# Kernel tuning notes

Measured on AMD Instinct MI355X. Metric: run time of the kernel, lower is better.

The kernel has to match this reference:

```python
import jax, jax.numpy as jnp
import numpy as np

EPS = 1e-5

def _lin(x, w, b):
    return x @ w + b

def _ln(x, scale, bias):
    m = jnp.mean(x, axis=-1, keepdims=True)
    v = jnp.var(x, axis=-1, keepdims=True)
    return (x - m) / jnp.sqrt(v + EPS) * scale + bias

def setup_inputs() -> dict:
    key = jax.random.key(0)
    B, N, F, OUT, TRI = 4, 128, 128, 128, 8
    ks = iter(jax.random.split(key, 64))
    def lin_params(fan_in, fan_out):
        s = 1.0 / np.sqrt(fan_in)
        w = jax.random.uniform(next(ks), (fan_in, fan_out), minval=-s, maxval=s, dtype=jnp.float32)
        b = jax.random.uniform(next(ks), (fan_out,), minval=-s, maxval=s, dtype=jnp.float32)
        return w, b
    inp = {}
    inp['node_fts'] = jax.random.normal(next(ks), (B, N, F), dtype=jnp.float32)
    inp['edge_fts'] = jax.random.normal(next(ks), (B, N, N, F), dtype=jnp.float32)
    inp['graph_fts'] = jax.random.normal(next(ks), (B, F), dtype=jnp.float32)
    inp['hidden'] = jax.random.normal(next(ks), (B, N, F), dtype=jnp.float32)
    inp['adj_matrix'] = jax.random.randint(next(ks), (B, N, N), 0, 2, dtype=jnp.int32)
    inp['m1_w'], inp['m1_b'] = lin_params(2 * F, OUT)
    inp['m2_w'], inp['m2_b'] = lin_params(2 * F, OUT)
    inp['me_w'], inp['me_b'] = lin_params(F, OUT)
    inp['mg_w'], inp['mg_b'] = lin_params(F, OUT)
    inp['mlp1_w'], inp['mlp1_b'] = lin_params(OUT, OUT)
    inp['mlp2_w'], inp['mlp2_b'] = lin_params(OUT, OUT)
    inp['o1_w'], inp['o1_b'] = lin_params(2 * F, OUT)
    inp['o2_w'], inp['o2_b'] = lin_params(OUT, OUT)
    inp['t1_w'], inp['t1_b'] = lin_params(2 * F, TRI)
    inp['t2_w'], inp['t2_b'] = lin_params(2 * F, TRI)
    inp['te1_w'], inp['te1_b'] = lin_params(F, TRI)
    inp['te2_w'], inp['te2_b'] = lin_params(F, TRI)
    inp['te3_w'], inp['te3_b'] = lin_params(F, TRI)
    inp['tg_w'], inp['tg_b'] = lin_params(F, TRI)
    inp['o3_w'], inp['o3_b'] = lin_params(TRI, OUT)
    inp['norm_scale'] = jnp.ones((OUT,), dtype=jnp.float32)
    inp['norm_bias'] = jnp.zeros((OUT,), dtype=jnp.float32)
    return inp

def reference(node_fts, edge_fts, graph_fts, hidden, adj_matrix,
              m1_w, m1_b, m2_w, m2_b, me_w, me_b, mg_w, mg_b,
              mlp1_w, mlp1_b, mlp2_w, mlp2_b,
              o1_w, o1_b, o2_w, o2_b,
              t1_w, t1_b, t2_w, t2_b,
              te1_w, te1_b, te2_w, te2_b, te3_w, te3_b,
              tg_w, tg_b, o3_w, o3_b, norm_scale, norm_bias):
    z = jnp.concatenate([node_fts, hidden], axis=-1)          # [B,N,2F]
    msg_1 = _lin(z, m1_w, m1_b)                                # [B,N,H]
    msg_2 = _lin(z, m2_w, m2_b)
    msg_e = _lin(edge_fts, me_w, me_b)                         # [B,N,N,H]
    msg_g = _lin(graph_fts, mg_w, mg_b)                        # [B,H]
    msgs = msg_1[:, None, :, :] + msg_2[:, :, None, :] + msg_e + msg_g[:, None, None, :]
    # msg_mlp: ReLU -> Linear -> ReLU -> Linear
    msgs = _lin(jax.nn.relu(_lin(jax.nn.relu(msgs), mlp1_w, mlp1_b)), mlp2_w, mlp2_b)
    # triplet messages (note: original code reuses t_1 for tri_3 -- faithful)
    tri_1 = _lin(z, t1_w, t1_b)                                # [B,N,T]
    tri_2 = _lin(z, t2_w, t2_b)
    tri_3 = _lin(z, t1_w, t1_b)
    tri_e_1 = _lin(edge_fts, te1_w, te1_b)                     # [B,N,N,T]
    tri_e_2 = _lin(edge_fts, te2_w, te2_b)
    tri_e_3 = _lin(edge_fts, te3_w, te3_b)
    tri_g = _lin(graph_fts, tg_w, tg_b)                        # [B,T]
    triplets = (tri_1[:, :, None, None, :] + tri_2[:, None, :, None, :]
                + tri_3[:, None, None, :, :]
                + tri_e_1[:, :, :, None, :] + tri_e_2[:, :, None, :, :]
                + tri_e_3[:, None, :, :, :]
                + tri_g[:, None, None, None, :])               # [B,N,N,N,T]
    tri_msgs = _lin(jnp.max(triplets, axis=1), o3_w, o3_b)     # [B,N,N,OUT]
    tri_msgs = _ln(jax.nn.relu(tri_msgs), norm_scale, norm_bias)
    # masked max aggregation
    maxarg = jnp.where(adj_matrix[..., None] == 1, msgs, -1e9)
    msgs_agg = jnp.max(maxarg, axis=1)                         # [B,N,H]
    out = jax.nn.relu(_lin(z, o1_w, o1_b) + _lin(msgs_agg, o2_w, o2_b))
    out = _ln(out, norm_scale, norm_bias)
    return out, tri_msgs
```

## Files before the change

### kernel.cpp

```cpp
#include <hip/hip_runtime.h>
#include <hip/hip_bf16.h>
#include <cstddef>
#include <cstdint>
#include <cstring>

typedef __attribute__((ext_vector_type(8))) short bf16x8;
typedef __attribute__((ext_vector_type(4))) float f32x4;
typedef unsigned short ushort_t;

__device__ __forceinline__ ushort_t f2b(float f) {
    uint32_t x = __float_as_uint(f);
    uint32_t r = (x + 0x7FFFu + ((x >> 16) & 1u)) >> 16;
    return (ushort_t)r;
}
__device__ __forceinline__ float b2f(ushort_t u) {
    return __uint_as_float(((uint32_t)u) << 16);
}
__device__ __forceinline__ uint32_t pk2(float x, float y) {
    __hip_bfloat162 h = __float22bfloat162_rn(float2{x, y});
    uint32_t u;
    __builtin_memcpy(&u, &h, 4);
    return u;
}

__global__ void prep_kernel(const float* __restrict__ m1_w, const float* __restrict__ m2_w,
                            const float* __restrict__ o1_w, const float* __restrict__ t1_w,
                            const float* __restrict__ t2_w,
                            const float* __restrict__ me_w, const float* __restrict__ mlp1_w,
                            const float* __restrict__ mlp2_w,
                            const float* __restrict__ te1_w, const float* __restrict__ te2_w,
                            const float* __restrict__ te3_w,
                            const float* __restrict__ graph_fts,
                            const float* __restrict__ mg_w, const float* __restrict__ mg_b,
                            const float* __restrict__ m1_b,
                            const float* __restrict__ tg_w, const float* __restrict__ t2_b,
                            const float* __restrict__ tg_b,
                            ushort_t* __restrict__ Wnt,
                            ushort_t* __restrict__ Wme, ushort_t* __restrict__ Wm1,
                            ushort_t* __restrict__ Wm2, ushort_t* __restrict__ TEt,
                            float* __restrict__ G1, float* __restrict__ TG) {
    int idx = blockIdx.x * 256 + threadIdx.x;
    if (idx < 106496) {
        int o = idx >> 8, k = idx & 255;
        float v = 0.0f;
        if (o < 128)       v = m1_w[k * 128 + o];
        else if (o < 256)  v = m2_w[k * 128 + (o - 128)];
        else if (o < 384)  v = o1_w[k * 128 + (o - 256)];
        else if (o < 392)  v = t1_w[k * 8 + (o - 384)];
        else if (o < 400)  v = t2_w[k * 8 + (o - 392)];
        Wnt[idx] = f2b(v);
    } else if (idx < 122880) {
        int t = idx - 106496, o = t >> 7, h = t & 127;
        Wme[t] = f2b(me_w[h * 128 + o]);
    } else if (idx < 139264) {
        int t = idx - 122880, o = t >> 7, h = t & 127;
        Wm1[t] = f2b(mlp1_w[h * 128 + o]);
    } else if (idx < 155648) {
        int t = idx - 139264, o = t >> 7, h = t & 127;
        Wm2[t] = f2b(mlp2_w[h * 128 + o]);
    } else if (idx < 159744) {
        int t = idx - 155648, c = t >> 7, h = t & 127;
        float v = 0.0f;
        if (c < 8)       v = te1_w[h * 8 + c];
        else if (c < 16) v = te2_w[h * 8 + (c - 8)];
        else if (c < 24) v = te3_w[h * 8 + (c - 16)];
        TEt[t] = f2b(v);
    } else if (idx < 160256) {
        int t = idx - 159744, b = t >> 7, h = t & 127;
        float a = m1_b[h] + mg_b[h];
        #pragma unroll 4
        for (int k = 0; k < 128; k++) a = fmaf(graph_fts[b * 128 + k], mg_w[k * 128 + h], a);
        G1[t] = a;
    } else if (idx < 160288) {
        int t = idx - 160256, b = t >> 3, tt = t & 7;
        float a = t2_b[tt] + tg_b[tt];
        #pragma unroll 4
        for (int k = 0; k < 128; k++) a = fmaf(graph_fts[b * 128 + k], tg_w[k * 8 + tt], a);
        TG[t] = a;
    }
}

__global__ __launch_bounds__(256)
void node_gemm(const float* __restrict__ node_fts, const float* __restrict__ hidden,
               const ushort_t* __restrict__ Wnt,
               const float* __restrict__ G1, const float* __restrict__ m2_b,
               const float* __restrict__ o1_b, const float* __restrict__ t1_b,
               const float* __restrict__ TG,
               float* __restrict__ M1, float* __restrict__ M2, float* __restrict__ O1z,
               float* __restrict__ T1v, float* __restrict__ TT2) {
    __shared__ ushort_t Zs[32 * 256];
    char* Zb = (char*)Zs;
    const int tid = threadIdx.x;
    const int blk = blockIdx.x;
    const int b = blk >> 2, q = blk & 3;
    const int row0 = b * 128 + q * 32;
    const int w = tid >> 6, l = tid & 63, g = l >> 4, lq = l & 15;

    const float4* nsrc = reinterpret_cast<const float4*>(node_fts + (size_t)row0 * 128);
    const float4* hsrc = reinterpret_cast<const float4*>(hidden + (size_t)row0 * 128);
    #pragma unroll
    for (int p = 0; p < 8; p++) {
        int idx = tid + p * 256;
        int r = idx >> 6, c4 = idx & 63;
        float4 v = (c4 < 32) ? nsrc[r * 32 + c4] : hsrc[r * 32 + (c4 - 32)];
        uint2 pk;
        pk.x = pk2(v.x, v.y);
        pk.y = pk2(v.z, v.w);
        *reinterpret_cast<uint2*>(Zb + r * 512 + (((c4 >> 1) ^ (r & 7)) << 4) + (c4 & 1) * 8) = pk;
    }
    __syncthreads();

    for (int mt = w; mt < 26; mt += 4) {
        f32x4 acc0 = (f32x4){0.f, 0.f, 0.f, 0.f};
        f32x4 acc1 = (f32x4){0.f, 0.f, 0.f, 0.f};
        const ushort_t* arow = Wnt + (size_t)(mt * 16 + lq) * 256;
        #pragma unroll
        for (int ks = 0; ks < 8; ks++) {
            bf16x8 a = *reinterpret_cast<const bf16x8*>(arow + ks * 32 + g * 8);
            int j0 = lq, j1 = 16 + lq;
            bf16x8 b0 = *reinterpret_cast<const bf16x8*>(Zb + j0 * 512 + (((ks * 4 + g) ^ (j0 & 7)) << 4));
            bf16x8 b1 = *reinterpret_cast<const bf16x8*>(Zb + j1 * 512 + (((ks * 4 + g) ^ (j1 & 7)) << 4));
            acc0 = __builtin_amdgcn_mfma_f32_16x16x32_bf16(a, b0, acc0, 0, 0, 0);
            acc1 = __builtin_amdgcn_mfma_f32_16x16x32_bf16(a, b1, acc1, 0, 0, 0);
        }
        #pragma unroll
        for (int half = 0; half < 2; half++) {
            const f32x4 acc = half ? acc1 : acc0;
            const int grow = row0 + half * 16 + lq;
            #pragma unroll
            for (int c = 0; c < 4; c++) {
                int o = mt * 16 + g * 4 + c;
                float v = acc[c];
                if (o < 128)       M1[(size_t)grow * 128 + o] = v + G1[b * 128 + o];
                else if (o < 256)  M2[(size_t)grow * 128 + (o - 128)] = v + m2_b[o - 128];
                else if (o < 384)  O1z[(size_t)grow * 128 + (o - 256)] = v + o1_b[o - 256];
                else if (o < 392)  T1v[(size_t)grow * 8 + (o - 384)] = v + t1_b[o - 384];
                else if (o < 400)  TT2[(size_t)grow * 8 + (o - 392)] = v + TG[b * 8 + (o - 392)];
            }
        }
    }
}

__device__ __forceinline__ void mmv(const ushort_t* __restrict__ Wt, const char* Xa,
                                    f32x4 acc[2][4], int o_blk, int j_blk, int g, int lq) {
    #pragma unroll
    for (int ks = 0; ks < 4; ks++) {
        bf16x8 a[2], bb[4];
        #pragma unroll
        for (int m = 0; m < 2; m++)
            a[m] = *reinterpret_cast<const bf16x8*>(Wt + (size_t)(o_blk + m * 16 + lq) * 128 + ks * 32 + g * 8);
        #pragma unroll
        for (int n = 0; n < 4; n++) {
            int j = j_blk + n * 16 + lq;
            bb[n] = *reinterpret_cast<const bf16x8*>(Xa + j * 256 + (((ks * 4 + g) ^ (j & 7)) << 4));
        }
        #pragma unroll
        for (int m = 0; m < 2; m++)
            #pragma unroll
            for (int n = 0; n < 4; n++)
                acc[m][n] = __builtin_amdgcn_mfma_f32_16x16x32_bf16(a[m], bb[n], acc[m][n], 0, 0, 0);
    }
}

__global__ __launch_bounds__(512, 4)
void edge_kernel(const float* __restrict__ edge_fts,
                 const ushort_t* __restrict__ Wme, const float* __restrict__ me_b,
                 const ushort_t* __restrict__ Wm1, const float* __restrict__ mlp1_b,
                 const ushort_t* __restrict__ Wm2, const float* __restrict__ mlp2_b,
                 const ushort_t* __restrict__ TEt,
                 const float* __restrict__ te1_b, const float* __restrict__ te2_b,
                 const float* __restrict__ te3_b,
                 const float* __restrict__ M1,  const float* __restrict__ M2,
                 const float* __restrict__ T1v, const float* __restrict__ TT2,
                 ushort_t* __restrict__ msgsM, float* __restrict__ T1buf,
                 float* __restrict__ T2buf, float* __restrict__ E3buf) {
    __shared__ ushort_t Xs[2][16384];
    char* X0 = (char*)Xs[0];
    char* X1 = (char*)Xs[1];
    const int tid = threadIdx.x;
    const int b  = blockIdx.x >> 7;
    const int ie = blockIdx.x & 127;
    const int w = tid >> 6, l = tid & 63, g = l >> 4, lq = l & 15;
    const int o_blk = (w & 3) * 32, j_blk = (w >> 2) * 64;

    const float4* esrc = reinterpret_cast<const float4*>(edge_fts + (size_t)(b * 128 + ie) * 16384);
    #pragma unroll
    for (int p = 0; p < 8; p++) {
        int idx = tid + p * 512;
        int r = idx >> 5, c4 = idx & 31;
        float4 v = esrc[idx];
        uint2 pk;
        pk.x = pk2(v.x, v.y);
        pk.y = pk2(v.z, v.w);
        *reinterpret_cast<uint2*>(X0 + r * 256 + (((c4 >> 1) ^ (r & 7)) << 4) + (c4 & 1) * 8) = pk;
    }
    __syncthreads();

    {
        const int m_te = w & 1;
        const int jq = (w >> 1) & 3;
        const ushort_t* At = TEt + m_te * 16 * 128;
        f32x4 acc2[2];
        #pragma unroll
        for (int n = 0; n < 2; n++) acc2[n] = (f32x4){0.f, 0.f, 0.f, 0.f};
        #pragma unroll
        for (int ks = 0; ks < 4; ks++) {
            bf16x8 a = *reinterpret_cast<const bf16x8*>(At + lq * 128 + ks * 32 + g * 8);
            #pragma unroll
            for (int n = 0; n < 2; n++) {
                int j = jq * 32 + n * 16 + lq;
                bf16x8 bbv = *reinterpret_cast<const bf16x8*>(X0 + j * 256 + (((ks * 4 + g) ^ (j & 7)) << 4));
                acc2[n] = __builtin_amdgcn_mfma_f32_16x16x32_bf16(a, bbv, acc2[n], 0, 0, 0);
            }
        }
        if (m_te == 0) {
            if (g < 2) {
                int t0 = g * 4;
                const float4 eb = *reinterpret_cast<const float4*>(te1_b + t0);
                const float4 tv = *reinterpret_cast<const float4*>(T1v + (size_t)(b * 128 + ie) * 8 + t0);
                #pragma unroll
                for (int n = 0; n < 2; n++) {
                    int j = jq * 32 + n * 16 + lq;
                    float4 o4 = make_float4(acc2[n][0] + eb.x + tv.x, acc2[n][1] + eb.y + tv.y,
                                            acc2[n][2] + eb.z + tv.z, acc2[n][3] + eb.w + tv.w);
                    *reinterpret_cast<float4*>(T1buf + ((size_t)(b * 128 + j) * 128 + ie) * 8 + t0) = o4;
                }
            } else {
                int t0 = g * 4 - 8;
                const float4 eb = *reinterpret_cast<const float4*>(te2_b + t0);
                #pragma unroll
                for (int n = 0; n < 2; n++) {
                    int j = jq * 32 + n * 16 + lq;
                    float4 o4 = make_float4(acc2[n][0] + eb.x, acc2[n][1] + eb.y,
                                            acc2[n][2] + eb.z, acc2[n][3] + eb.w);
                    *reinterpret_cast<float4*>(T2buf + ((size_t)(b * 128 + ie) * 128 + j) * 8 + t0) = o4;
                }
            }
        } else if (g < 2) {
            int t0 = g * 4;
            const float4 eb = *reinterpret_cast<const float4*>(te3_b + t0);
            const float4 t2v = *reinterpret_cast<const float4*>(TT2 + (size_t)(b * 128 + ie) * 8 + t0);
            #pragma unroll
            for (int n = 0; n < 2; n++) {
                int j = jq * 32 + n * 16 + lq;
                const float4 t3v = *reinterpret_cast<const float4*>(T1v + (size_t)(b * 128 + j) * 8 + t0);
                float4 o4 = make_float4(acc2[n][0] + eb.x + t2v.x + t3v.x,
                                        acc2[n][1] + eb.y + t2v.y + t3v.y,
                                        acc2[n][2] + eb.z + t2v.z + t3v.z,
                                        acc2[n][3] + eb.w + t2v.w + t3v.w);
                *reinterpret_cast<float4*>(E3buf + ((size_t)(b * 128 + ie) * 128 + j) * 8 + t0) = o4;
            }
        }
    }

    f32x4 acc[2][4];

    #pragma unroll
    for (int m = 0; m < 2; m++)
        #pragma unroll
        for (int n = 0; n < 4; n++) acc[m][n] = (f32x4){0.f, 0.f, 0.f, 0.f};
    mmv(Wme, X0, acc, o_blk, j_blk, g, lq);
    {
        #pragma unroll
        for (int m = 0; m < 2; m++) {
            int o0 = o_blk + m * 16 + g * 4;
            const float4 eb = *reinterpret_cast<const float4*>(me_b + o0);
            const float4 m2 = *reinterpret_cast<const float4*>(M2 + (size_t)(b * 128 + ie) * 128 + o0);
            float4 bc = make_float4(eb.x + m2.x, eb.y + m2.y, eb.z + m2.z, eb.w + m2.w);
            #pragma unroll
            for (int n = 0; n < 4; n++) {
                int j = j_blk + n * 16 + lq;
                const float4 m1 = *reinterpret_cast<const float4*>(M1 + (size_t)(b * 128 + j) * 128 + o0);
                float r0 = fmaxf(acc[m][n][0] + bc.x + m1.x, 0.f);
                float r1 = fmaxf(acc[m][n][1] + bc.y + m1.y, 0.f);
                float r2 = fmaxf(acc[m][n][2] + bc.z + m1.z, 0.f);
                float r3 = fmaxf(acc[m][n][3] + bc.w + m1.w, 0.f);
                uint2 pk;
                pk.x = pk2(r0, r1);
                pk.y = pk2(r2, r3);
                *reinterpret_cast<uint2*>(X1 + j * 256 + ((((o0 >> 3) ^ (j & 7))) << 4) + (o0 & 7) * 2) = pk;
            }
        }
        __syncthreads();
    }

    #pragma unroll
    for (int m = 0; m < 2; m++)
        #pragma unroll
        for (int n = 0; n < 4; n++) acc[m][n] = (f32x4){0.f, 0.f, 0.f, 0.f};
    mmv(Wm1, X1, acc, o_blk, j_blk, g, lq);
    {
        #pragma unroll
        for (int m = 0; m < 2; m++) {
            int o0 = o_blk + m * 16 + g * 4;
            const float4 bb = *reinterpret_cast<const float4*>(mlp1_b + o0);
            #pragma unroll
            for (int n = 0; n < 4; n++) {
                int j = j_blk + n * 16 + lq;
                float r0 = fmaxf(acc[m][n][0] + bb.x, 0.f);
                float r1 = fmaxf(acc[m][n][1] + bb.y, 0.f);
                float r2 = fmaxf(acc[m][n][2] + bb.z, 0.f);
                float r3 = fmaxf(acc[m][n][3] + bb.w, 0.f);
                uint2 pk;
                pk.x = pk2(r0, r1);
                pk.y = pk2(r2, r3);
                *reinterpret_cast<uint2*>(X0 + j * 256 + ((((o0 >> 3) ^ (j & 7))) << 4) + (o0 & 7) * 2) = pk;
            }
        }
        __syncthreads();
    }

    #pragma unroll
    for (int m = 0; m < 2; m++)
        #pragma unroll
        for (int n = 0; n < 4; n++) acc[m][n] = (f32x4){0.f, 0.f, 0.f, 0.f};
    mmv(Wm2, X0, acc, o_blk, j_blk, g, lq);
    {
        #pragma unroll
        for (int m = 0; m < 2; m++) {
            int o0 = o_blk + m * 16 + g * 4;
            const float4 bb = *reinterpret_cast<const float4*>(mlp2_b + o0);
            #pragma unroll
            for (int n = 0; n < 4; n++) {
                int j = j_blk + n * 16 + lq;
                float r0 = acc[m][n][0] + bb.x;
                float r1 = acc[m][n][1] + bb.y;
                float r2 = acc[m][n][2] + bb.z;
                float r3 = acc[m][n][3] + bb.w;
                uint2 pk;
                pk.x = pk2(r0, r1);
                pk.y = pk2(r2, r3);
                *reinterpret_cast<uint2*>(X1 + j * 256 + ((((o0 >> 3) ^ (j & 7))) << 4) + (o0 & 7) * 2) = pk;
            }
        }
        __syncthreads();
    }

    {
        #pragma unroll
        for (int p = 0; p < 4; p++) {
            int idx = tid + p * 512;
            int r = idx >> 4, sc = idx & 15;
            uint4 v = *reinterpret_cast<const uint4*>(X1 + r * 256 + sc * 16);
            int logical = sc ^ (r & 7);
            *reinterpret_cast<uint4*>(msgsM + ((size_t)(b * 128 + r) * 128 + ie) * 128 + logical * 8) = v;
        }
    }
}

__global__ __launch_bounds__(256)
void agg_out_kernel(const ushort_t* __restrict__ msgsM, const int* __restrict__ adj,
                    const float* __restrict__ O1z,
                    const float* __restrict__ o2_w, const float* __restrict__ o2_b,
                    const float* __restrict__ scale, const float* __restrict__ bias,
                    float* __restrict__ out) {
    __shared__ float aggs[4][128];
    __shared__ float fagg[128];
    __shared__ float red[2][2];
    const int b = blockIdx.x >> 7, j = blockIdx.x & 127;
    const int t = threadIdx.x;
    const int wv = t >> 6, ln = t & 63;
    const ushort_t* msrc = msgsM + (size_t)(b * 128 + j) * 16384;
    const int* arow = adj + b * 16384 + j;
    float a0 = -1e9f, a1 = -1e9f;
    #pragma unroll 8
    for (int s = 0; s < 32; s++) {
        const int i = s * 4 + wv;
        uint32_t u = *reinterpret_cast<const uint32_t*>(msrc + i * 128 + ln * 2);
        bool m = (arow[i * 128] == 1);
        float x0 = b2f((ushort_t)(u & 0xffffu));
        float x1 = b2f((ushort_t)(u >> 16));
        a0 = m ? fmaxf(a0, x0) : a0;
        a1 = m ? fmaxf(a1, x1) : a1;
    }
    aggs[wv][ln * 2]     = a0;
    aggs[wv][ln * 2 + 1] = a1;
    __syncthreads();
    if (t < 128)
        fagg[t] = fmaxf(fmaxf(aggs[0][t], aggs[1][t]), fmaxf(aggs[2][t], aggs[3][t]));
    __syncthreads();

    float v = 0.0f;
    if (t < 128) {
        float val = o2_b[t] + O1z[(size_t)(b * 128 + j) * 128 + t];
        #pragma unroll 4
        for (int k = 0; k < 128; k++) val = fmaf(fagg[k], o2_w[k * 128 + t], val);
        v = fmaxf(val, 0.0f);
    }
    float s = v, s2 = v * v;
    #pragma unroll
    for (int off = 32; off >= 1; off >>= 1) {
        s += __shfl_down(s, off, 64);
        s2 += __shfl_down(s2, off, 64);
    }
    if (t < 128 && (t & 63) == 0) { red[t >> 6][0] = s; red[t >> 6][1] = s2; }
    __syncthreads();
    if (t < 128) {
        const float tot = red[0][0] + red[1][0];
        const float tot2 = red[0][1] + red[1][1];
        const float mean = tot * (1.0f / 128.0f);
        const float var = tot2 * (1.0f / 128.0f) - mean * mean;
        const float rstd = rsqrtf(var + 1e-5f);
        out[(size_t)(b * 128 + j) * 128 + t] = (v - mean) * rstd * scale[t] + bias[t];
    }
}

__global__ __launch_bounds__(512)
void tri_kernel(const float* __restrict__ T1buf, const float* __restrict__ T2buf,
                const float* __restrict__ E3buf, const float* __restrict__ o3_w,
                const float* __restrict__ o3_b, const float* __restrict__ scale,
                const float* __restrict__ bias, float* __restrict__ tri_out) {
    __shared__ __align__(16) float T1s[1024];
    __shared__ __align__(16) float E3s[1024];
    __shared__ __align__(16) float o3s[1024];
    __shared__ __align__(16) float Ps[4][128][8];
    const int b = blockIdx.x >> 7, jf = blockIdx.x & 127;
    const int tid = threadIdx.x;
    if (tid < 256) {
        reinterpret_cast<float4*>(T1s)[tid] =
            reinterpret_cast<const float4*>(T1buf + (size_t)(b * 128 + jf) * 1024)[tid];
        reinterpret_cast<float4*>(o3s)[tid] = reinterpret_cast<const float4*>(o3_w)[tid];
    } else {
        int t2 = tid - 256;
        reinterpret_cast<float4*>(E3s)[t2] =
            reinterpret_cast<const float4*>(E3buf + (size_t)(b * 128 + jf) * 1024)[t2];
    }
    __syncthreads();

    {
        const int kf = tid & 127, ih = tid >> 7;
        float a8[8];
        #pragma unroll
        for (int t = 0; t < 8; t++) a8[t] = -3.0e38f;
        const float4* t2p = reinterpret_cast<const float4*>(T2buf + (size_t)b * 131072);
        #pragma unroll 4
        for (int ii = 0; ii < 32; ++ii) {
            const int i = ih * 32 + ii;
            const float4 p = t2p[(i * 128 + kf) * 2];
            const float4 q = t2p[(i * 128 + kf) * 2 + 1];
            const float* t1r = &T1s[i * 8];
            a8[0] = fmaxf(a8[0], t1r[0] + p.x);
            a8[1] = fmaxf(a8[1], t1r[1] + p.y);
            a8[2] = fmaxf(a8[2], t1r[2] + p.z);
            a8[3] = fmaxf(a8[3], t1r[3] + p.w);
            a8[4] = fmaxf(a8[4], t1r[4] + q.x);
            a8[5] = fmaxf(a8[5], t1r[5] + q.y);
            a8[6] = fmaxf(a8[6], t1r[6] + q.z);
            a8[7] = fmaxf(a8[7], t1r[7] + q.w);
        }
        #pragma unroll
        for (int t = 0; t < 8; t++) Ps[ih][kf][t] = a8[t];
    }
    __syncthreads();

    const int w = tid >> 6, l = tid & 63;
    const float ob0 = o3_b[l],     ob1 = o3_b[l + 64];
    const float sc0 = scale[l],    sc1 = scale[l + 64];
    const float bi0 = bias[l],     bi1 = bias[l + 64];
    for (int kk = 0; kk < 16; ++kk) {
        const int kf = w * 16 + kk;
        float m8[8];
        #pragma unroll
        for (int t = 0; t < 8; t++)
            m8[t] = fmaxf(fmaxf(Ps[0][kf][t], Ps[1][kf][t]),
                          fmaxf(Ps[2][kf][t], Ps[3][kf][t])) + E3s[kf * 8 + t];
        float v0 = ob0, v1 = ob1;
        #pragma unroll
        for (int t = 0; t < 8; t++) {
            v0 = fmaf(m8[t], o3s[t * 128 + l], v0);
            v1 = fmaf(m8[t], o3s[t * 128 + l + 64], v1);
        }
        v0 = fmaxf(v0, 0.0f);
        v1 = fmaxf(v1, 0.0f);
        float s = v0 + v1, s2 = v0 * v0 + v1 * v1;
        #pragma unroll
        for (int off = 32; off >= 1; off >>= 1) {
            s  += __shfl_xor(s, off, 64);
            s2 += __shfl_xor(s2, off, 64);
        }
        const float mean = s * (1.0f / 128.0f);
        const float var = s2 * (1.0f / 128.0f) - mean * mean;
        const float rstd = rsqrtf(var + 1e-5f);
        float* dst = tri_out + (size_t)((b * 128 + jf) * 128 + kf) * 128;
        dst[l]      = (v0 - mean) * rstd * sc0 + bi0;
        dst[l + 64] = (v1 - mean) * rstd * sc1 + bi1;
    }
}

extern "C" void kernel_launch(void* const* d_in, const int* in_sizes, int n_in,
                              void* d_out, int out_size, void* d_ws, size_t ws_size,
                              hipStream_t stream) {
    const float* node_fts  = (const float*)d_in[0];
    const float* edge_fts  = (const float*)d_in[1];
    const float* graph_fts = (const float*)d_in[2];
    const float* hidden    = (const float*)d_in[3];
    const int*   adj       = (const int*)d_in[4];
    const float* m1_w = (const float*)d_in[5],  *m1_b = (const float*)d_in[6];
    const float* m2_w = (const float*)d_in[7],  *m2_b = (const float*)d_in[8];
    const float* me_w = (const float*)d_in[9],  *me_b = (const float*)d_in[10];
    const float* mg_w = (const float*)d_in[11], *mg_b = (const float*)d_in[12];
    const float* mlp1_w = (const float*)d_in[13], *mlp1_b = (const float*)d_in[14];
    const float* mlp2_w = (const float*)d_in[15], *mlp2_b = (const float*)d_in[16];
    const float* o1_w = (const float*)d_in[17], *o1_b = (const float*)d_in[18];
    const float* o2_w = (const float*)d_in[19], *o2_b = (const float*)d_in[20];
    const float* t1_w = (const float*)d_in[21], *t1_b = (const float*)d_in[22];
    const float* t2_w = (const float*)d_in[23], *t2_b = (const float*)d_in[24];
    const float* te1_w = (const float*)d_in[25], *te1_b = (const float*)d_in[26];
    const float* te2_w = (const float*)d_in[27], *te2_b = (const float*)d_in[28];
    const float* te3_w = (const float*)d_in[29], *te3_b = (const float*)d_in[30];
    const float* tg_w = (const float*)d_in[31], *tg_b = (const float*)d_in[32];
    const float* o3_w = (const float*)d_in[33], *o3_b = (const float*)d_in[34];
    const float* norm_scale = (const float*)d_in[35];
    const float* norm_bias  = (const float*)d_in[36];

    char* w8 = (char*)d_ws;
    float*    M1    = (float*)(w8 + 0);
    float*    M2    = (float*)(w8 + 262144);
    float*    O1z   = (float*)(w8 + 524288);
    float*    T1v   = (float*)(w8 + 786432);
    float*    TT2   = (float*)(w8 + 802816);
    ushort_t* Wme   = (ushort_t*)(w8 + 819200);
    ushort_t* Wm1   = (ushort_t*)(w8 + 851968);
    ushort_t* Wm2   = (ushort_t*)(w8 + 884736);
    ushort_t* TEt   = (ushort_t*)(w8 + 917504);
    ushort_t* msgsM = (ushort_t*)(w8 + 925696);
    float*    T1buf = (float*)(w8 + 17702912);
    float*    T2buf = (float*)(w8 + 19800064);
    float*    E3buf = (float*)(w8 + 21897216);
    ushort_t* Wnt   = (ushort_t*)(w8 + 23994368);
    float*    G1    = (float*)(w8 + 24207360);
    float*    TG    = (float*)(w8 + 24209408);

    float* out_p  = (float*)d_out;
    float* tri_p  = (float*)d_out + 65536;

    prep_kernel<<<627, 256, 0, stream>>>(m1_w, m2_w, o1_w, t1_w, t2_w,
                                         me_w, mlp1_w, mlp2_w, te1_w, te2_w, te3_w,
                                         graph_fts, mg_w, mg_b, m1_b, tg_w, t2_b, tg_b,
                                         Wnt, Wme, Wm1, Wm2, TEt, G1, TG);
    node_gemm<<<16, 256, 0, stream>>>(node_fts, hidden, Wnt, G1, m2_b, o1_b, t1_b, TG,
                                      M1, M2, O1z, T1v, TT2);
    edge_kernel<<<512, 512, 0, stream>>>(edge_fts, Wme, me_b, Wm1, mlp1_b, Wm2, mlp2_b,
                                         TEt, te1_b, te2_b, te3_b,
                                         M1, M2, T1v, TT2, msgsM, T1buf, T2buf, E3buf);
    agg_out_kernel<<<512, 256, 0, stream>>>(msgsM, adj, O1z, o2_w, o2_b,
                                            norm_scale, norm_bias, out_p);
    tri_kernel<<<512, 512, 0, stream>>>(T1buf, T2buf, E3buf, o3_w, o3_b,
                                        norm_scale, norm_bias, tri_p);
}
```

Measured before the change: 109.8 us.

## Fuse masked max aggregation and output layer into edge kernel via column-major edge tiling

Each edge_kernel block now handles one target column jf across all source rows i instead of one source row. The block therefore holds every message needed for the masked max over i in shared memory. It runs the aggregation, the o2 projection and the layernorm in place, which removes the 16 MB bf16 msgs round trip to global memory and the separate agg_out launch. Edge feature loads become strided per row (512 B chunks), and node_gemm is split into twice as many blocks across output-column halves for more parallelism.

```diff
diff --git a/kernel.cpp b/kernel.cpp
--- a/kernel.cpp
+++ b/kernel.cpp
@@ -92,7 +92,8 @@
     char* Zb = (char*)Zs;
     const int tid = threadIdx.x;
     const int blk = blockIdx.x;
-    const int b = blk >> 2, q = blk & 3;
+    const int rowblk = blk >> 1, colh = blk & 1;
+    const int b = rowblk >> 2, q = rowblk & 3;
     const int row0 = b * 128 + q * 32;
     const int w = tid >> 6, l = tid & 63, g = l >> 4, lq = l & 15;
 
@@ -110,7 +111,7 @@
     }
     __syncthreads();
 
-    for (int mt = w; mt < 26; mt += 4) {
+    for (int mt = colh * 13 + w; mt < colh * 13 + 13; mt += 4) {
         f32x4 acc0 = (f32x4){0.f, 0.f, 0.f, 0.f};
         f32x4 acc1 = (f32x4){0.f, 0.f, 0.f, 0.f};
         const ushort_t* arow = Wnt + (size_t)(mt * 16 + lq) * 256;
@@ -172,23 +173,28 @@
                  const float* __restrict__ te3_b,
                  const float* __restrict__ M1,  const float* __restrict__ M2,
                  const float* __restrict__ T1v, const float* __restrict__ TT2,
-                 ushort_t* __restrict__ msgsM, float* __restrict__ T1buf,
-                 float* __restrict__ T2buf, float* __restrict__ E3buf) {
+                 const int* __restrict__ adj, const float* __restrict__ O1z,
+                 const float* __restrict__ o2_w, const float* __restrict__ o2_b,
+                 const float* __restrict__ nsc, const float* __restrict__ nbi,
+                 float* __restrict__ out,
+                 float* __restrict__ T1buf, float* __restrict__ T2buf,
+                 float* __restrict__ E3buf) {
     __shared__ ushort_t Xs[2][16384];
     char* X0 = (char*)Xs[0];
     char* X1 = (char*)Xs[1];
     const int tid = threadIdx.x;
     const int b  = blockIdx.x >> 7;
-    const int ie = blockIdx.x & 127;
+    const int jf = blockIdx.x & 127;
     const int w = tid >> 6, l = tid & 63, g = l >> 4, lq = l & 15;
     const int o_blk = (w & 3) * 32, j_blk = (w >> 2) * 64;
 
-    const float4* esrc = reinterpret_cast<const float4*>(edge_fts + (size_t)(b * 128 + ie) * 16384);
     #pragma unroll
     for (int p = 0; p < 8; p++) {
         int idx = tid + p * 512;
         int r = idx >> 5, c4 = idx & 31;
-        float4 v = esrc[idx];
+        const float4* src = reinterpret_cast<const float4*>(
+            edge_fts + ((size_t)(b * 128 + r) * 128 + jf) * 128);
+        float4 v = src[c4];
         uint2 pk;
         pk.x = pk2(v.x, v.y);
         pk.y = pk2(v.z, v.w);
@@ -217,38 +223,38 @@
             if (g < 2) {
                 int t0 = g * 4;
                 const float4 eb = *reinterpret_cast<const float4*>(te1_b + t0);
-                const float4 tv = *reinterpret_cast<const float4*>(T1v + (size_t)(b * 128 + ie) * 8 + t0);
                 #pragma unroll
                 for (int n = 0; n < 2; n++) {
-                    int j = jq * 32 + n * 16 + lq;
+                    int r = jq * 32 + n * 16 + lq;
+                    const float4 tv = *reinterpret_cast<const float4*>(T1v + (size_t)(b * 128 + r) * 8 + t0);
                     float4 o4 = make_float4(acc2[n][0] + eb.x + tv.x, acc2[n][1] + eb.y + tv.y,
                                             acc2[n][2] + eb.z + tv.z, acc2[n][3] + eb.w + tv.w);
-                    *reinterpret_cast<float4*>(T1buf + ((size_t)(b * 128 + j) * 128 + ie) * 8 + t0) = o4;
+                    *reinterpret_cast<float4*>(T1buf + ((size_t)(b * 128 + jf) * 128 + r) * 8 + t0) = o4;
                 }
             } else {
                 int t0 = g * 4 - 8;
                 const float4 eb = *reinterpret_cast<const float4*>(te2_b + t0);
                 #pragma unroll
                 for (int n = 0; n < 2; n++) {
-                    int j = jq * 32 + n * 16 + lq;
+                    int r = jq * 32 + n * 16 + lq;
                     float4 o4 = make_float4(acc2[n][0] + eb.x, acc2[n][1] + eb.y,
                                             acc2[n][2] + eb.z, acc2[n][3] + eb.w);
-                    *reinterpret_cast<float4*>(T2buf + ((size_t)(b * 128 + ie) * 128 + j) * 8 + t0) = o4;
+                    *reinterpret_cast<float4*>(T2buf + ((size_t)(b * 128 + r) * 128 + jf) * 8 + t0) = o4;
                 }
             }
         } else if (g < 2) {
             int t0 = g * 4;
             const float4 eb = *reinterpret_cast<const float4*>(te3_b + t0);
-            const float4 t2v = *reinterpret_cast<const float4*>(TT2 + (size_t)(b * 128 + ie) * 8 + t0);
+            const float4 t3v = *reinterpret_cast<const float4*>(T1v + (size_t)(b * 128 + jf) * 8 + t0);
             #pragma unroll
             for (int n = 0; n < 2; n++) {
-                int j = jq * 32 + n * 16 + lq;
-                const float4 t3v = *reinterpret_cast<const float4*>(T1v + (size_t)(b * 128 + j) * 8 + t0);
+                int r = jq * 32 + n * 16 + lq;
+                const float4 t2v = *reinterpret_cast<const float4*>(TT2 + (size_t)(b * 128 + r) * 8 + t0);
                 float4 o4 = make_float4(acc2[n][0] + eb.x + t2v.x + t3v.x,
                                         acc2[n][1] + eb.y + t2v.y + t3v.y,
                                         acc2[n][2] + eb.z + t2v.z + t3v.z,
                                         acc2[n][3] + eb.w + t2v.w + t3v.w);
-                *reinterpret_cast<float4*>(E3buf + ((size_t)(b * 128 + ie) * 128 + j) * 8 + t0) = o4;
+                *reinterpret_cast<float4*>(E3buf + ((size_t)(b * 128 + r) * 128 + jf) * 8 + t0) = o4;
             }
         }
     }
@@ -265,16 +271,16 @@
         for (int m = 0; m < 2; m++) {
             int o0 = o_blk + m * 16 + g * 4;
             const float4 eb = *reinterpret_cast<const float4*>(me_b + o0);
-            const float4 m2 = *reinterpret_cast<const float4*>(M2 + (size_t)(b * 128 + ie) * 128 + o0);
-            float4 bc = make_float4(eb.x + m2.x, eb.y + m2.y, eb.z + m2.z, eb.w + m2.w);
+            const float4 m1 = *reinterpret_cast<const float4*>(M1 + (size_t)(b * 128 + jf) * 128 + o0);
+            float4 bc = make_float4(eb.x + m1.x, eb.y + m1.y, eb.z + m1.z, eb.w + m1.w);
             #pragma unroll
             for (int n = 0; n < 4; n++) {
                 int j = j_blk + n * 16 + lq;
-                const float4 m1 = *reinterpret_cast<const float4*>(M1 + (size_t)(b * 128 + j) * 128 + o0);
-                float r0 = fmaxf(acc[m][n][0] + bc.x + m1.x, 0.f);
-                float r1 = fmaxf(acc[m][n][1] + bc.y + m1.y, 0.f);
-                float r2 = fmaxf(acc[m][n][2] + bc.z + m1.z, 0.f);
-                float r3 = fmaxf(acc[m][n][3] + bc.w + m1.w, 0.f);
+                const float4 m2 = *reinterpret_cast<const float4*>(M2 + (size_t)(b * 128 + j) * 128 + o0);
+                float r0 = fmaxf(acc[m][n][0] + bc.x + m2.x, 0.f);
+                float r1 = fmaxf(acc[m][n][1] + bc.y + m2.y, 0.f);
+                float r2 = fmaxf(acc[m][n][2] + bc.z + m2.z, 0.f);
+                float r3 = fmaxf(acc[m][n][3] + bc.w + m2.w, 0.f);
                 uint2 pk;
                 pk.x = pk2(r0, r1);
                 pk.y = pk2(r2, r3);
@@ -337,71 +343,59 @@
     }
 
     {
-        #pragma unroll
-        for (int p = 0; p < 4; p++) {
-            int idx = tid + p * 512;
-            int r = idx >> 4, sc = idx & 15;
-            uint4 v = *reinterpret_cast<const uint4*>(X1 + r * 256 + sc * 16);
-            int logical = sc ^ (r & 7);
-            *reinterpret_cast<uint4*>(msgsM + ((size_t)(b * 128 + r) * 128 + ie) * 128 + logical * 8) = v;
-        }
-    }
-}
-
-__global__ __launch_bounds__(256)
-void agg_out_kernel(const ushort_t* __restrict__ msgsM, const int* __restrict__ adj,
-                    const float* __restrict__ O1z,
-                    const float* __restrict__ o2_w, const float* __restrict__ o2_b,
-                    const float* __restrict__ scale, const float* __restrict__ bias,
-                    float* __restrict__ out) {
-    __shared__ float aggs[4][128];
-    __shared__ float fagg[128];
-    __shared__ float red[2][2];
-    const int b = blockIdx.x >> 7, j = blockIdx.x & 127;
-    const int t = threadIdx.x;
-    const int wv = t >> 6, ln = t & 63;
-    const ushort_t* msrc = msgsM + (size_t)(b * 128 + j) * 16384;
-    const int* arow = adj + b * 16384 + j;
-    float a0 = -1e9f, a1 = -1e9f;
-    #pragma unroll 8
-    for (int s = 0; s < 32; s++) {
-        const int i = s * 4 + wv;
-        uint32_t u = *reinterpret_cast<const uint32_t*>(msrc + i * 128 + ln * 2);
-        bool m = (arow[i * 128] == 1);
-        float x0 = b2f((ushort_t)(u & 0xffffu));
-        float x1 = b2f((ushort_t)(u >> 16));
-        a0 = m ? fmaxf(a0, x0) : a0;
-        a1 = m ? fmaxf(a1, x1) : a1;
-    }
-    aggs[wv][ln * 2]     = a0;
-    aggs[wv][ln * 2 + 1] = a1;
-    __syncthreads();
-    if (t < 128)
-        fagg[t] = fmaxf(fmaxf(aggs[0][t], aggs[1][t]), fmaxf(aggs[2][t], aggs[3][t]));
-    __syncthreads();
-
-    float v = 0.0f;
-    if (t < 128) {
-        float val = o2_b[t] + O1z[(size_t)(b * 128 + j) * 128 + t];
-        #pragma unroll 4
-        for (int k = 0; k < 128; k++) val = fmaf(fagg[k], o2_w[k * 128 + t], val);
-        v = fmaxf(val, 0.0f);
-    }
-    float s = v, s2 = v * v;
-    #pragma unroll
-    for (int off = 32; off >= 1; off >>= 1) {
-        s += __shfl_down(s, off, 64);
-        s2 += __shfl_down(s2, off, 64);
-    }
-    if (t < 128 && (t & 63) == 0) { red[t >> 6][0] = s; red[t >> 6][1] = s2; }
-    __syncthreads();
-    if (t < 128) {
-        const float tot = red[0][0] + red[1][0];
-        const float tot2 = red[0][1] + red[1][1];
-        const float mean = tot * (1.0f / 128.0f);
-        const float var = tot2 * (1.0f / 128.0f) - mean * mean;
-        const float rstd = rsqrtf(var + 1e-5f);
-        out[(size_t)(b * 128 + j) * 128 + t] = (v - mean) * rstd * scale[t] + bias[t];
+        float* scr  = reinterpret_cast<float*>(X0);
+        float* aggs = scr;
+        float* fagg = scr + 512;
+        float* sums = scr + 640;
+        float* red  = scr + 1152;
+        const int h = tid & 127, wv = tid >> 7;
+        {
+            const int* acol = adj + b * 16384 + jf;
+            float amax = -1e9f;
+            #pragma unroll 8
+            for (int s = 0; s < 32; s++) {
+                int r = wv * 32 + s;
+                ushort_t u = *reinterpret_cast<const ushort_t*>(
+                    X1 + r * 256 + (((h >> 3) ^ (r & 7)) << 4) + (h & 7) * 2);
+                amax = (acol[r * 128] == 1) ? fmaxf(amax, b2f(u)) : amax;
+            }
+            aggs[wv * 128 + h] = amax;
+        }
+        __syncthreads();
+        if (tid < 128)
+            fagg[tid] = fmaxf(fmaxf(aggs[tid], aggs[128 + tid]),
+                              fmaxf(aggs[256 + tid], aggs[384 + tid]));
+        __syncthreads();
+        {
+            float part = 0.f;
+            const float* wcol = o2_w + h;
+            #pragma unroll 8
+            for (int k = wv * 32; k < wv * 32 + 32; k++)
+                part = fmaf(fagg[k], wcol[k * 128], part);
+            sums[wv * 128 + h] = part;
+        }
+        __syncthreads();
+        float v = 0.f;
+        if (tid < 128) {
+            float val = o2_b[h] + O1z[(size_t)(b * 128 + jf) * 128 + h]
+                      + sums[h] + sums[128 + h] + sums[256 + h] + sums[384 + h];
+            v = fmaxf(val, 0.f);
+        }
+        float s = v, s2 = v * v;
+        #pragma unroll
+        for (int off = 32; off >= 1; off >>= 1) {
+            s  += __shfl_down(s, off, 64);
+            s2 += __shfl_down(s2, off, 64);
+        }
+        if (tid < 128 && (tid & 63) == 0) { red[tid >> 6] = s; red[2 + (tid >> 6)] = s2; }
+        __syncthreads();
+        if (tid < 128) {
+            const float tot = red[0] + red[1], tot2 = red[2] + red[3];
+            const float mean = tot * (1.0f / 128.0f);
+            const float var = tot2 * (1.0f / 128.0f) - mean * mean;
+            const float rstd = rsqrtf(var + 1e-5f);
+            out[(size_t)(b * 128 + jf) * 128 + h] = (v - mean) * rstd * nsc[h] + nbi[h];
+        }
     }
 }
 
@@ -523,7 +517,6 @@
     ushort_t* Wm1   = (ushort_t*)(w8 + 851968);
     ushort_t* Wm2   = (ushort_t*)(w8 + 884736);
     ushort_t* TEt   = (ushort_t*)(w8 + 917504);
-    ushort_t* msgsM = (ushort_t*)(w8 + 925696);
     float*    T1buf = (float*)(w8 + 17702912);
     float*    T2buf = (float*)(w8 + 19800064);
     float*    E3buf = (float*)(w8 + 21897216);
@@ -538,13 +531,13 @@
                                          me_w, mlp1_w, mlp2_w, te1_w, te2_w, te3_w,
                                          graph_fts, mg_w, mg_b, m1_b, tg_w, t2_b, tg_b,
                                          Wnt, Wme, Wm1, Wm2, TEt, G1, TG);
-    node_gemm<<<16, 256, 0, stream>>>(node_fts, hidden, Wnt, G1, m2_b, o1_b, t1_b, TG,
+    node_gemm<<<32, 256, 0, stream>>>(node_fts, hidden, Wnt, G1, m2_b, o1_b, t1_b, TG,
                                       M1, M2, O1z, T1v, TT2);
     edge_kernel<<<512, 512, 0, stream>>>(edge_fts, Wme, me_b, Wm1, mlp1_b, Wm2, mlp2_b,
                                          TEt, te1_b, te2_b, te3_b,
-                                         M1, M2, T1v, TT2, msgsM, T1buf, T2buf, E3buf);
-    agg_out_kernel<<<512, 256, 0, stream>>>(msgsM, adj, O1z, o2_w, o2_b,
-                                            norm_scale, norm_bias, out_p);
+                                         M1, M2, T1v, TT2,
+                                         adj, O1z, o2_w, o2_b, norm_scale, norm_bias,
+                                         out_p, T1buf, T2buf, E3buf);
     tri_kernel<<<512, 512, 0, stream>>>(T1buf, T2buf, E3buf, o3_w, o3_b,
                                         norm_scale, norm_bias, tri_p);
 }
```

Result: faster. 93.99 us (-14.4%).
